# Optimization experiments

Measured on AMD Instinct MI355X. Metric: run time of the kernel, lower is better.

The kernel has to match this reference:

```python
import jax, jax.numpy as jnp
import numpy as np

K = 11          # k_size in the original module
HALF = K // 2   # 5
N_SIGNAL = 33554432  # 2**25 elements, 128 MB fp32


def setup_inputs() -> dict:
    key = jax.random.key(0)
    k1, _ = jax.random.split(key)
    x = jax.random.normal(k1, (N_SIGNAL,), dtype=jnp.float32)
    # learned parameter of Dilation1D(s=1.5)
    scale = jnp.asarray(1.5, dtype=jnp.float32)
    return {"x": x, "scale": scale}


def reference(x, scale):
    # parabolic structuring element: z = -5..5, h = -z^2 / (4*scale)
    z = jnp.linspace(-(K // 2), K // 2, K, dtype=jnp.float32)  # torch: -k//2+1 .. k//2 == -5..5
    h = -(z * z) / (4.0 * scale)  # [K]

    n = x.shape[0]
    pad = jnp.full((HALF,), -jnp.inf, dtype=x.dtype)
    xp = jnp.concatenate([pad, x, pad])  # [n + K - 1], -inf edge handling == original branches

    # out[r] = max_j ( x[r - HALF + j] + h[j] )  (max-plus / grayscale dilation)
    out = xp[0:n] + h[0]
    for j in range(1, K):  # fixed small K, unrolled window — no data-dim loop
        out = jnp.maximum(out, xp[j:j + n] + h[j])
    return out
```

## Files before the change

kernel.cpp:

```cpp
#include <hip/hip_runtime.h>
#include <math.h>


#define KSZ  11
#define HALF 5
#define ITER 4

__global__ __launch_bounds__(256) void dilate1d_kernel(
    const float4* __restrict__ x4,
    const float*  __restrict__ scale_p,
    float4*       __restrict__ out4,
    int n4)
{
    const float s = scale_p[0];
    float h[KSZ];
#pragma unroll
    for (int j = 0; j < KSZ; ++j) {
        float z = (float)(j - HALF);
        h[j] = -(z * z) / (4.0f * s);
    }

    const float NEG = -INFINITY;
    const int stride = gridDim.x * blockDim.x;

    for (int q = blockIdx.x * blockDim.x + threadIdx.x; q < n4; q += stride) {
        float xs[20];

        if (q >= 2 && q + 2 < n4) {
#pragma unroll
            for (int t = 0; t < 5; ++t) {
                float4 v = x4[q - 2 + t];
                xs[4 * t + 0] = v.x;
                xs[4 * t + 1] = v.y;
                xs[4 * t + 2] = v.z;
                xs[4 * t + 3] = v.w;
            }
        } else {
#pragma unroll
            for (int t = 0; t < 5; ++t) {
                int qq = q - 2 + t;
                float4 v;
                if (qq >= 0 && qq < n4) v = x4[qq];
                else                    v = make_float4(NEG, NEG, NEG, NEG);
                xs[4 * t + 0] = v.x;
                xs[4 * t + 1] = v.y;
                xs[4 * t + 2] = v.z;
                xs[4 * t + 3] = v.w;
            }
        }

        float4 o;
        float* op = &o.x;
#pragma unroll
        for (int i = 0; i < 4; ++i) {
            int c = 8 + i;
            float m = xs[c - HALF] + h[0];
#pragma unroll
            for (int j = 1; j < KSZ; ++j) {
                m = fmaxf(m, xs[c - HALF + j] + h[j]);
            }
            op[i] = m;
        }
        out4[q] = o;
    }
}

extern "C" void kernel_launch(void* const* d_in, const int* in_sizes, int n_in,
                              void* d_out, int out_size, void* d_ws, size_t ws_size,
                              hipStream_t stream) {
    const float* x       = (const float*)d_in[0];
    const float* scale_p = (const float*)d_in[1];
    float*       out     = (float*)d_out;

    int n  = in_sizes[0];
    int n4 = n / 4;

    int block = 256;
    long long threads_wanted = (long long)(n4 + ITER - 1) / ITER;
    int grid = (int)((threads_wanted + block - 1) / block);

    dilate1d_kernel<<<grid, block, 0, stream>>>(
        (const float4*)x, scale_p, (float4*)out, n4);
}
```

Baseline: 231.1 us.

## Stage input tile with halo in shared memory and exploit symmetric kernel

```diff
diff --git a/kernel.cpp b/kernel.cpp
--- a/kernel.cpp
+++ b/kernel.cpp
@@ -2,51 +2,72 @@
 #include <math.h>
 
 
-#define KSZ  11
-#define HALF 5
-#define ITER 4
+#define BLOCK   256
+#define QPT     4
+#define TILE_Q  (BLOCK * QPT)
+#define HALO_Q  2
+#define STAGE_Q (TILE_Q + 2 * HALO_Q)
 
-__global__ __launch_bounds__(256) void dilate1d_kernel(
+__global__ __launch_bounds__(BLOCK) void dilate1d_kernel(
     const float4* __restrict__ x4,
     const float*  __restrict__ scale_p,
     float4*       __restrict__ out4,
     int n4)
 {
-    const float s = scale_p[0];
-    float h[KSZ];
+    __shared__ float4 smem[STAGE_Q];
+
+    const float NEG  = -INFINITY;
+    const float4 NEG4 = make_float4(NEG, NEG, NEG, NEG);
+
+    const int Q0 = blockIdx.x * TILE_Q;
+    const int g0 = Q0 - HALO_Q;
+
+    const bool interior = (g0 >= 0) && (g0 + STAGE_Q <= n4);
+    if (interior) {
 #pragma unroll
-    for (int j = 0; j < KSZ; ++j) {
-        float z = (float)(j - HALF);
-        h[j] = -(z * z) / (4.0f * s);
+        for (int t = 0; t < QPT; ++t) {
+            int idx = threadIdx.x + t * BLOCK;
+            smem[idx] = x4[g0 + idx];
+        }
+        if (threadIdx.x < 2 * HALO_Q) {
+            int idx = TILE_Q + threadIdx.x;
+            smem[idx] = x4[g0 + idx];
+        }
+    } else {
+#pragma unroll
+        for (int t = 0; t <= QPT; ++t) {
+            int idx = threadIdx.x + t * BLOCK;
+            if (idx < STAGE_Q) {
+                int g = g0 + idx;
+                smem[idx] = (g >= 0 && g < n4) ? x4[g] : NEG4;
+            }
+        }
     }
+    __syncthreads();
 
-    const float NEG = -INFINITY;
-    const int stride = gridDim.x * blockDim.x;
+    const float r4s = 1.0f / (4.0f * scale_p[0]);
+    float hparr[6];
+    hparr[0] = 0.0f;
+    hparr[1] = -1.0f  * r4s;
+    hparr[2] = -4.0f  * r4s;
+    hparr[3] = -9.0f  * r4s;
+    hparr[4] = -16.0f * r4s;
+    hparr[5] = -25.0f * r4s;
 
-    for (int q = blockIdx.x * blockDim.x + threadIdx.x; q < n4; q += stride) {
-        float xs[20];
+#pragma unroll
+    for (int t = 0; t < QPT; ++t) {
+        int idx = threadIdx.x + t * BLOCK;
+        int q   = Q0 + idx;
+        if (q >= n4) break;
 
-        if (q >= 2 && q + 2 < n4) {
+        float w[20];
 #pragma unroll
-            for (int t = 0; t < 5; ++t) {
-                float4 v = x4[q - 2 + t];
-                xs[4 * t + 0] = v.x;
-                xs[4 * t + 1] = v.y;
-                xs[4 * t + 2] = v.z;
-                xs[4 * t + 3] = v.w;
-            }
-        } else {
-#pragma unroll
-            for (int t = 0; t < 5; ++t) {
-                int qq = q - 2 + t;
-                float4 v;
-                if (qq >= 0 && qq < n4) v = x4[qq];
-                else                    v = make_float4(NEG, NEG, NEG, NEG);
-                xs[4 * t + 0] = v.x;
-                xs[4 * t + 1] = v.y;
-                xs[4 * t + 2] = v.z;
-                xs[4 * t + 3] = v.w;
-            }
+        for (int r = 0; r < 5; ++r) {
+            float4 v = smem[idx + r];
+            w[4 * r + 0] = v.x;
+            w[4 * r + 1] = v.y;
+            w[4 * r + 2] = v.z;
+            w[4 * r + 3] = v.w;
         }
 
         float4 o;
@@ -54,10 +75,10 @@
 #pragma unroll
         for (int i = 0; i < 4; ++i) {
             int c = 8 + i;
-            float m = xs[c - HALF] + h[0];
+            float m = w[c];
 #pragma unroll
-            for (int j = 1; j < KSZ; ++j) {
-                m = fmaxf(m, xs[c - HALF + j] + h[j]);
+            for (int d = 1; d <= 5; ++d) {
+                m = fmaxf(m, hparr[d] + fmaxf(w[c - d], w[c + d]));
             }
             op[i] = m;
         }
@@ -75,10 +96,8 @@
     int n  = in_sizes[0];
     int n4 = n / 4;
 
-    int block = 256;
-    long long threads_wanted = (long long)(n4 + ITER - 1) / ITER;
-    int grid = (int)((threads_wanted + block - 1) / block);
+    int grid = (n4 + TILE_Q - 1) / TILE_Q;
 
-    dilate1d_kernel<<<grid, block, 0, stream>>>(
+    dilate1d_kernel<<<grid, BLOCK, 0, stream>>>(
         (const float4*)x, scale_p, (float4*)out, n4);
 }
```

New measurement: 229.7 us. About the same (-0.6%).
